# Kernel optimization log

Measured on AMD Instinct MI355X. Metric: run time of the kernel, lower is better.

Reference implementation:

```python
import math
import jax, jax.numpy as jnp
import numpy as np

N, T, C, V = 32, 2048, 512, 500


def setup_inputs() -> dict:
    key = jax.random.key(0)
    k1, k2, k3 = jax.random.split(key, 3)
    x = jax.random.normal(k1, (N, T, C), dtype=jnp.float32)
    x_lens = jax.random.randint(k2, (N,), 0, T, dtype=jnp.int64)
    ctc_output = jax.random.normal(k3, (N, T, V), dtype=jnp.float32)
    return {"x": x, "x_lens": x_lens, "ctc_output": ctc_output, "blank_id": 0}


def reference(x, x_lens, ctc_output, blank_id):
    # x: [N, T, C]; ctc_output: [N, T, V]; x_lens: [N]
    n, t, c = x.shape
    frame_idx = jnp.arange(t)  # [T]
    padding_mask = frame_idx[None, :] >= x_lens[:, None]              # [N, T]
    left = ctc_output[:, :, blank_id] < math.log(0.9)                 # blank posterior threshold
    non_blank_mask = left & (~padding_mask)                           # [N, T]
    out_lens = non_blank_mask.sum(axis=1)                             # [N]

    # Stable compaction: sort keep-frames (False < True on discard flag)
    # to the front of each row, preserving temporal order.
    order = jnp.argsort(~non_blank_mask, axis=1, stable=True)         # [N, T]
    out = jnp.take_along_axis(x, order[:, :, None], axis=1)           # [N, T, C]

    # Zero positions past each row's reduced length (original pads with zeros).
    valid = frame_idx[None, :] < out_lens[:, None]                    # [N, T]
    out = out * valid[:, :, None].astype(x.dtype)
    # Note: kept static-padded to T (jit-safe); original slices to out_lens.max().
    return out, out_lens
```

## Files before the change

kernel.cpp:

```cpp
#include <hip/hip_runtime.h>
#include <hip/hip_bf16.h>

#define RN 32
#define RT 2048
#define RC 512
#define RV 500

#define LOG09 (-0.10536052f)

__global__ void fr_flags(const float* __restrict__ ctc,
                         const int* __restrict__ x_lens,
                         const int* __restrict__ blank_id_p,
                         unsigned long long* __restrict__ flag_words)
{
    const int g = blockIdx.x * 256 + threadIdx.x;
    const int n = g >> 11;
    const int t = g & (RT - 1);
    const int blank = blank_id_p[0];

    const bool keep = (t < x_lens[n]) &&
                      (ctc[(size_t)g * RV + blank] < LOG09);
    const unsigned long long b = __ballot(keep);
    if ((threadIdx.x & 63) == 0) {
        flag_words[g >> 6] = b;
    }
}

__global__ void fr_scan(const unsigned long long* __restrict__ flag_words,
                        int* __restrict__ src_idx,
                        int* __restrict__ lens_i,
                        float* __restrict__ lens_f)
{
    const int n    = blockIdx.x;
    const int lane = threadIdx.x;

    unsigned long long word = 0;
    int cnt = 0;
    if (lane < 32) {
        word = flag_words[n * 32 + lane];
        cnt  = __popcll(word);
    }

    int incl = cnt;
#pragma unroll
    for (int off = 1; off < 32; off <<= 1) {
        int v = __shfl_up(incl, off, 64);
        if (lane >= off) incl += v;
    }
    const int total = __shfl(incl, 31, 64);

    if (lane < 32) {
        int pos = incl - cnt;
        int* srow = src_idx + n * RT;
        const int base = lane * 64;
        unsigned long long w = word;
        while (w) {
            const int j = __ffsll((long long)w) - 1;
            srow[pos++] = base + j;
            w &= w - 1;
        }
    }
    if (lane == 0) {
        lens_i[n] = total;
        lens_f[n] = (float)total;
    }
}

__global__ void fr_gather(const float* __restrict__ x,
                          const int* __restrict__ src_idx,
                          const int* __restrict__ lens_i,
                          float4* __restrict__ out)
{
    const int r    = blockIdx.x * 2 + (threadIdx.x >> 7);
    const int lane = threadIdx.x & 127;
    const int n = r >> 11;
    const int p = r & (RT - 1);

    float4 v = make_float4(0.f, 0.f, 0.f, 0.f);
    if (p < lens_i[n]) {
        const int t = src_idx[n * RT + p];
        const float4* xr = (const float4*)(x + ((size_t)n * RT + t) * RC);
        v = xr[lane];
    }
    out[(size_t)r * (RC / 4) + lane] = v;
}

extern "C" void kernel_launch(void* const* d_in, const int* in_sizes, int n_in,
                              void* d_out, int out_size, void* d_ws, size_t ws_size,
                              hipStream_t stream) {
    const float* x        = (const float*)d_in[0];
    const int*   x_lens   = (const int*)d_in[1];
    const float* ctc      = (const float*)d_in[2];
    const int*   blank_id = (const int*)d_in[3];

    float* out    = (float*)d_out;
    float* lens_f = out + (size_t)RN * RT * RC;

    int* src_idx = (int*)d_ws;
    int* lens_i  = src_idx + RN * RT;
    unsigned long long* flag_words =
        (unsigned long long*)(lens_i + RN + (RN & 1));

    fr_flags<<<(RN * RT) / 256, 256, 0, stream>>>(ctc, x_lens, blank_id, flag_words);
    fr_scan<<<RN, 64, 0, stream>>>(flag_words, src_idx, lens_i, lens_f);
    fr_gather<<<(RN * RT) / 2, 256, 0, stream>>>(x, src_idx, lens_i, (float4*)out);
}
```

Before: 36.13 us.

## Fuse per-row scan into gather kernel, computing source indices per block

Removes the separate single-wave scan kernel and its src_idx workspace round-trip. Each gather block now redoes the 32-word prefix scan over the row's flag words and binary-searches the word and bit position for each of its 32 output rows. Blocks each cover 32 rows instead of 2, so the launch is smaller and each thread issues 16 float4 loads. The cost is redundant scan work in every block and two block-level barriers before the copy starts.

```diff
diff --git a/kernel.cpp b/kernel.cpp
--- a/kernel.cpp
+++ b/kernel.cpp
@@ -8,10 +8,12 @@
 
 #define LOG09 (-0.10536052f)
 
+typedef unsigned long long ull;
+
 __global__ void fr_flags(const float* __restrict__ ctc,
                          const int* __restrict__ x_lens,
                          const int* __restrict__ blank_id_p,
-                         unsigned long long* __restrict__ flag_words)
+                         ull* __restrict__ flag_words)
 {
     const int g = blockIdx.x * 256 + threadIdx.x;
     const int n = g >> 11;
@@ -20,69 +22,83 @@
 
     const bool keep = (t < x_lens[n]) &&
                       (ctc[(size_t)g * RV + blank] < LOG09);
-    const unsigned long long b = __ballot(keep);
+    const ull b = __ballot(keep);
     if ((threadIdx.x & 63) == 0) {
         flag_words[g >> 6] = b;
     }
 }
 
-__global__ void fr_scan(const unsigned long long* __restrict__ flag_words,
-                        int* __restrict__ src_idx,
-                        int* __restrict__ lens_i,
-                        float* __restrict__ lens_f)
+__global__ void fr_gather(const float* __restrict__ x,
+                          const ull* __restrict__ flag_words,
+                          float* __restrict__ out,
+                          float* __restrict__ lens_f)
 {
-    const int n    = blockIdx.x;
-    const int lane = threadIdx.x;
+    const int blk    = blockIdx.x;
+    const int n      = blk >> 6;
+    const int base_p = (blk & 63) * 32;
+    const int tid    = threadIdx.x;
 
-    unsigned long long word = 0;
-    int cnt = 0;
-    if (lane < 32) {
-        word = flag_words[n * 32 + lane];
-        cnt  = __popcll(word);
+    __shared__ ull sh_w[32];
+    __shared__ int sh_incl[32];
+    __shared__ int sh_t[32];
+    __shared__ int sh_total;
+
+    if (tid < 64) {
+        ull w = 0; int c = 0;
+        if (tid < 32) { w = flag_words[n * 32 + tid]; c = __popcll(w); }
+        int incl = c;
+#pragma unroll
+        for (int off = 1; off < 32; off <<= 1) {
+            int v = __shfl_up(incl, off, 64);
+            if (tid >= off) incl += v;
+        }
+        if (tid < 32) { sh_w[tid] = w; sh_incl[tid] = incl; }
+        if (tid == 31) sh_total = incl;
     }
+    __syncthreads();
 
-    int incl = cnt;
+    const int total = sh_total;
+    if (tid < 32) {
+        const int p = base_p + tid;
+        int t = -1;
+        if (p < total) {
+            int wi = 0;
 #pragma unroll
-    for (int off = 1; off < 32; off <<= 1) {
-        int v = __shfl_up(incl, off, 64);
-        if (lane >= off) incl += v;
+            for (int step = 16; step; step >>= 1) {
+                const int probe = wi + step - 1;
+                if (probe < 32 && sh_incl[probe] <= p) wi += step;
+            }
+            const int excl = (wi > 0) ? sh_incl[wi - 1] : 0;
+            int r = p - excl;
+            const ull w = sh_w[wi];
+            int pos = 0;
+#pragma unroll
+            for (int b = 32; b; b >>= 1) {
+                const ull m = ((1ull << b) - 1) << pos;
+                const int c2 = __popcll(w & m);
+                if (r >= c2) { r -= c2; pos += b; }
+            }
+            t = wi * 64 + pos;
+        }
+        sh_t[tid] = t;
     }
-    const int total = __shfl(incl, 31, 64);
+    if (base_p == 0 && tid == 31) {
+        lens_f[n] = (float)sh_total;
+    }
+    __syncthreads();
 
-    if (lane < 32) {
-        int pos = incl - cnt;
-        int* srow = src_idx + n * RT;
-        const int base = lane * 64;
-        unsigned long long w = word;
-        while (w) {
-            const int j = __ffsll((long long)w) - 1;
-            srow[pos++] = base + j;
-            w &= w - 1;
-        }
+    const float4* xbase = (const float4*)x + (size_t)n * RT * (RC / 4);
+    float4* outr = (float4*)out + ((size_t)(n * RT + base_p)) * (RC / 4);
+#pragma unroll
+    for (int i = 0; i < 16; ++i) {
+        const int idx  = i * 256 + tid;
+        const int rl   = idx >> 7;
+        const int lane = idx & 127;
+        const int t = sh_t[rl];
+        float4 v = make_float4(0.f, 0.f, 0.f, 0.f);
+        if (t >= 0) v = xbase[(size_t)t * (RC / 4) + lane];
+        outr[(size_t)rl * (RC / 4) + lane] = v;
     }
-    if (lane == 0) {
-        lens_i[n] = total;
-        lens_f[n] = (float)total;
-    }
-}
-
-__global__ void fr_gather(const float* __restrict__ x,
-                          const int* __restrict__ src_idx,
-                          const int* __restrict__ lens_i,
-                          float4* __restrict__ out)
-{
-    const int r    = blockIdx.x * 2 + (threadIdx.x >> 7);
-    const int lane = threadIdx.x & 127;
-    const int n = r >> 11;
-    const int p = r & (RT - 1);
-
-    float4 v = make_float4(0.f, 0.f, 0.f, 0.f);
-    if (p < lens_i[n]) {
-        const int t = src_idx[n * RT + p];
-        const float4* xr = (const float4*)(x + ((size_t)n * RT + t) * RC);
-        v = xr[lane];
-    }
-    out[(size_t)r * (RC / 4) + lane] = v;
 }
 
 extern "C" void kernel_launch(void* const* d_in, const int* in_sizes, int n_in,
@@ -96,12 +112,8 @@
     float* out    = (float*)d_out;
     float* lens_f = out + (size_t)RN * RT * RC;
 
-    int* src_idx = (int*)d_ws;
-    int* lens_i  = src_idx + RN * RT;
-    unsigned long long* flag_words =
-        (unsigned long long*)(lens_i + RN + (RN & 1));
+    ull* flag_words = (ull*)d_ws;
 
     fr_flags<<<(RN * RT) / 256, 256, 0, stream>>>(ctc, x_lens, blank_id, flag_words);
-    fr_scan<<<RN, 64, 0, stream>>>(flag_words, src_idx, lens_i, lens_f);
-    fr_gather<<<(RN * RT) / 2, 256, 0, stream>>>(x, src_idx, lens_i, (float4*)out);
+    fr_gather<<<(RN * RT) / 32, 256, 0, stream>>>(x, flag_words, out, lens_f);
 }
```

New measurement: 35.41 us. 1.02x faster.
